# Optimization experiments

Measured on AMD Instinct MI355X. Metric: run time of the kernel, lower is better.

The kernel has to match this reference:

```python
import jax, jax.numpy as jnp
import numpy as np

NEG_SLOPE = 0.2


def gat_conv(x, edge_index, W, a_src, a_dst, b, concat):
    """PyG-style GATConv: add self-loops, linear, edge attention, scatter-softmax, scatter-add."""
    N = x.shape[0]
    H, C = a_src.shape
    loop = jnp.arange(N)
    src = jnp.concatenate([edge_index[0], loop])  # source j (messages flow j -> i)
    dst = jnp.concatenate([edge_index[1], loop])  # target i (aggregation node)
    h = (x @ W).reshape(N, H, C)                  # [N,H,C]
    alpha_s = jnp.sum(h * a_src, axis=-1)         # [N,H]
    alpha_d = jnp.sum(h * a_dst, axis=-1)         # [N,H]
    e = jax.nn.leaky_relu(alpha_s[src] + alpha_d[dst], NEG_SLOPE)  # [E,H]
    # numerically stable scatter-softmax over edges grouped by destination node
    m = jax.ops.segment_max(e, dst, num_segments=N)                # [N,H]
    ex = jnp.exp(e - m[dst])
    denom = jax.ops.segment_sum(ex, dst, num_segments=N)           # [N,H]
    alpha = ex / (denom[dst] + 1e-16)                              # [E,H]
    out = jax.ops.segment_sum(h[src] * alpha[:, :, None], dst, num_segments=N)  # [N,H,C]
    out = out.reshape(N, H * C) if concat else out.mean(axis=1)
    return out + b


def setup_inputs() -> dict:
    key = jax.random.key(0)
    ks = jax.random.split(key, 12)
    N, E, F_IN, HID, OUT, HEADS = 100000, 1600000, 128, 128, 64, 4
    C1 = HID // HEADS
    x = jax.random.normal(ks[0], (N, F_IN), dtype=jnp.float32)
    edge_index = jax.random.randint(ks[1], (2, E), 0, N, dtype=jnp.int64)
    s = 0.05
    return {
        "x": x,
        "edge_index": edge_index,
        "W1": jax.random.normal(ks[2], (F_IN, HEADS * C1), dtype=jnp.float32) * s,
        "a_src1": jax.random.normal(ks[3], (HEADS, C1), dtype=jnp.float32) * s,
        "a_dst1": jax.random.normal(ks[4], (HEADS, C1), dtype=jnp.float32) * s,
        "b1": jnp.zeros((HEADS * C1,), dtype=jnp.float32),
        "W2": jax.random.normal(ks[5], (HID, OUT), dtype=jnp.float32) * s,
        "a_src2": jax.random.normal(ks[6], (1, OUT), dtype=jnp.float32) * s,
        "a_dst2": jax.random.normal(ks[7], (1, OUT), dtype=jnp.float32) * s,
        "b2": jnp.zeros((OUT,), dtype=jnp.float32),
    }


def reference(x, edge_index, W1, a_src1, a_dst1, b1, W2, a_src2, a_dst2, b2):
    h = jax.nn.elu(gat_conv(x, edge_index, W1, a_src1, a_dst1, b1, concat=True))
    # F.dropout(p=0.5, training=False) is the identity in eval mode
    out = gat_conv(h, edge_index, W2, a_src2, a_dst2, b2, concat=False)
    return out
```

## Files before the change

### kernel.cpp

```cpp
#include <hip/hip_runtime.h>
#include <hip/hip_fp16.h>
#include <math.h>
#include <string.h>


#define BSH 9
#define DPB 512
#define NBK 256
#define CH1 16384
#define DBINS 512
#define OCH 1024
#define HB 128
#define LOG2E 1.44269504088896f

using half8 = __attribute__((ext_vector_type(8))) _Float16;
using half4 = __attribute__((ext_vector_type(4))) _Float16;
using floatx4 = __attribute__((ext_vector_type(4))) float;

__device__ __forceinline__ float exp2_fast(float x) {
#if __has_builtin(__builtin_amdgcn_exp2f)
    return __builtin_amdgcn_exp2f(x);
#else
    return exp2f(x);
#endif
}

__device__ __forceinline__ void wfrag(const float* __restrict__ W, __half* __restrict__ WtF,
                                      int NC, int fid) {
    int col = fid & 15, quad = (fid >> 4) & 3, rest = fid >> 6;
    int NT = NC >> 4;
    int t = rest & (NT - 1), k0s = rest / NT;
    int n = t * 16 + col;
    int k = k0s * 32 + quad * 8;
#pragma unroll
    for (int j = 0; j < 8; ++j)
        WtF[fid * 8 + j] = __float2half(W[(k + j) * NC + n]);
}


__global__ __launch_bounds__(256) void bucket_hist(const int* __restrict__ ei, int E, int N,
                                                   unsigned* __restrict__ bcount,
                                                   const float* __restrict__ W1,
                                                   const float* __restrict__ W2,
                                                   __half* __restrict__ WtF1,
                                                   __half* __restrict__ WtF2) {
    if (blockIdx.x >= HB) {
        int tid = (blockIdx.x - HB) * 256 + threadIdx.x;
        if (tid < 2048) wfrag(W1, WtF1, 128, tid);
        else if (tid < 3072) wfrag(W2, WtF2, 64, tid - 2048);
        return;
    }
    __shared__ unsigned hist[NBK];
    int t = threadIdx.x;
    hist[t] = 0;
    __syncthreads();
    int Etot = E + N;
    for (int k = blockIdx.x * 256 + t; k < Etot; k += HB * 256) {
        int d = (k < E) ? ei[E + k] : (k - E);
        atomicAdd(&hist[d >> BSH], 1u);
    }
    __syncthreads();
    unsigned c = hist[t];
    if (c) atomicAdd(&bcount[t], c);
}

__global__ void scan_buckets(const unsigned* __restrict__ bcount, unsigned* __restrict__ bbase,
                             unsigned* __restrict__ bcursor) {
    __shared__ unsigned s[NBK];
    int t = threadIdx.x;
    unsigned v = bcount[t];
    s[t] = v;
    __syncthreads();
    for (int o = 1; o < NBK; o <<= 1) {
        unsigned add = (t >= o) ? s[t - o] : 0;
        __syncthreads();
        s[t] += add;
        __syncthreads();
    }
    unsigned excl = s[t] - v;
    bbase[t] = excl;
    bcursor[t] = excl;
    if (t == NBK - 1) bbase[NBK] = excl + v;
}

__global__ __launch_bounds__(256) void bucket_scatter(const int* __restrict__ ei, int E, int N,
                                                      unsigned* __restrict__ bcursor,
                                                      unsigned* __restrict__ rec) {
    __shared__ unsigned hist[NBK];
    __shared__ unsigned base[NBK];
    int t = threadIdx.x;
    hist[t] = 0;
    __syncthreads();
    int Etot = E + N;
    int k0 = blockIdx.x * CH1;
    int k1 = min(k0 + CH1, Etot);
    for (int k = k0 + t; k < k1; k += 256) {
        int d = (k < E) ? ei[E + k] : (k - E);
        atomicAdd(&hist[d >> BSH], 1u);
    }
    __syncthreads();
    unsigned c = hist[t];
    base[t] = c ? atomicAdd(&bcursor[t], c) : 0u;
    hist[t] = 0;
    __syncthreads();
    for (int k = k0 + t; k < k1; k += 256) {
        int s, d;
        if (k < E) { s = ei[k]; d = ei[E + k]; } else { s = d = k - E; }
        int b = d >> BSH;
        unsigned r = atomicAdd(&hist[b], 1u);
        rec[base[b] + r] = (unsigned)s | ((unsigned)(d & (DPB - 1)) << 17);
    }
}


__global__ __launch_bounds__(256) void bucket_sort(const unsigned* __restrict__ rec,
                                                   const unsigned* __restrict__ bbase,
                                                   int* __restrict__ offs, int* __restrict__ srcs,
                                                   unsigned* __restrict__ deghist,
                                                   unsigned* __restrict__ done,
                                                   unsigned* __restrict__ degcur,
                                                   int N, int Etot, int NSB) {
    __shared__ unsigned hist[DPB];
    __shared__ unsigned tsum[256];
    __shared__ unsigned deg_l[DBINS];
    int t = threadIdx.x, bb = blockIdx.x;
    unsigned r0 = bbase[bb], r1 = bbase[bb + 1];
    hist[t] = 0;
    hist[t + 256] = 0;
    deg_l[t] = 0;
    deg_l[t + 256] = 0;
    __syncthreads();
    int dlo = bb << BSH;
    for (unsigned k = r0 + t; k < r1; k += 256) {
        unsigned e = rec[k];
        atomicAdd(&hist[e >> 17], 1u);
    }
    __syncthreads();
    unsigned h0 = hist[2 * t], h1 = hist[2 * t + 1];
    int d0 = dlo + 2 * t;
    if (d0 < N) atomicAdd(&deg_l[min(h0, (unsigned)(DBINS - 1))], 1u);
    if (d0 + 1 < N) atomicAdd(&deg_l[min(h1, (unsigned)(DBINS - 1))], 1u);
    tsum[t] = h0 + h1;
    __syncthreads();
    for (int o = 1; o < 256; o <<= 1) {
        unsigned a = (t >= o) ? tsum[t - o] : 0;
        __syncthreads();
        tsum[t] += a;
        __syncthreads();
    }
    unsigned tb = tsum[t] - (h0 + h1);
    if (d0 < N) offs[d0] = (int)(r0 + tb);
    if (d0 + 1 < N) offs[d0 + 1] = (int)(r0 + tb + h0);
    hist[2 * t] = tb;
    hist[2 * t + 1] = tb + h0;
    __syncthreads();
    for (unsigned k = r0 + t; k < r1; k += 256) {
        unsigned e = rec[k];
        unsigned r = atomicAdd(&hist[e >> 17], 1u);
        srcs[r0 + r] = (int)(e & 0x1FFFFu);
    }
    if (bb == 0 && t == 0) offs[N] = Etot;
    unsigned c0 = deg_l[t], c1 = deg_l[t + 256];
    if (c0) atomicAdd(&deghist[t], c0);
    if (c1) atomicAdd(&deghist[t + 256], c1);
    __threadfence();
    __shared__ bool amlast;
    if (t == 0) amlast = (atomicAdd(done, 1u) == (unsigned)(NSB - 1));
    __syncthreads();
    if (!amlast) return;
    unsigned v0 = atomicAdd(&deghist[t], 0u);
    unsigned v1 = atomicAdd(&deghist[t + 256], 0u);
    deg_l[t] = v0;
    deg_l[t + 256] = v1;
    __syncthreads();
    for (int o = 1; o < DBINS; o <<= 1) {
        unsigned a0 = (t >= o) ? deg_l[t - o] : 0u;
        unsigned a1 = (t + 256 >= o) ? deg_l[t + 256 - o] : 0u;
        __syncthreads();
        deg_l[t] += a0;
        deg_l[t + 256] += a1;
        __syncthreads();
    }
    degcur[t] = deg_l[t] - v0;
    degcur[t + 256] = deg_l[t + 256] - v1;
}


__global__ __launch_bounds__(256) void order_scatter(const int* __restrict__ offs,
                                                     unsigned* __restrict__ degcur,
                                                     int* __restrict__ order, int N) {
    __shared__ unsigned hist[DBINS];
    __shared__ unsigned base[DBINS];
    int t = threadIdx.x;
    hist[t] = 0;
    hist[t + 256] = 0;
    __syncthreads();
    int k0 = blockIdx.x * OCH, k1 = min(k0 + OCH, N);
    for (int k = k0 + t; k < k1; k += 256) {
        int deg = offs[k + 1] - offs[k];
        atomicAdd(&hist[min(deg, DBINS - 1)], 1u);
    }
    __syncthreads();
    for (int i = t; i < DBINS; i += 256) {
        unsigned c = hist[i];
        base[i] = c ? atomicAdd(&degcur[i], c) : 0u;
        hist[i] = 0;
    }
    __syncthreads();
    for (int k = k0 + t; k < k1; k += 256) {
        int deg = offs[k + 1] - offs[k];
        int b = min(deg, DBINS - 1);
        unsigned r = atomicAdd(&hist[b], 1u);
        order[base[b] + r] = k;
    }
}


template <int NC, int H, typename InT>
__global__ __launch_bounds__(256) void gemm_mfma(const InT* __restrict__ A,
                                                 const __half* __restrict__ WtF,
                                                 __half* __restrict__ C,
                                                 const float* __restrict__ a_src,
                                                 const float* __restrict__ a_dst,
                                                 float* __restrict__ as,
                                                 float* __restrict__ ad, int M) {
    constexpr int NT = NC / 16;
    constexpr int TPH = NT / H;
    int wave = threadIdx.x >> 6;
    int lane = threadIdx.x & 63;
    int quad = lane >> 4, col = lane & 15;
    int row0 = blockIdx.x * 64 + wave * 16;
    int arow = row0 + col;
    if (arow >= M) arow = M - 1;
    floatx4 acc[NT] = {};
    const half8* wf = reinterpret_cast<const half8*>(WtF) + lane;
#pragma unroll
    for (int k0s = 0; k0s < 4; ++k0s) {
        int k0 = k0s * 32;
        half8 af;
        if constexpr (sizeof(InT) == 4) {
            const float* ap = (const float*)A + (size_t)arow * 128 + k0 + quad * 8;
            float4 v0 = *reinterpret_cast<const float4*>(ap);
            float4 v1 = *reinterpret_cast<const float4*>(ap + 4);
            af[0] = (_Float16)v0.x; af[1] = (_Float16)v0.y;
            af[2] = (_Float16)v0.z; af[3] = (_Float16)v0.w;
            af[4] = (_Float16)v1.x; af[5] = (_Float16)v1.y;
            af[6] = (_Float16)v1.z; af[7] = (_Float16)v1.w;
        } else {
            af = *reinterpret_cast<const half8*>((const __half*)A + (size_t)arow * 128 + k0 + quad * 8);
        }
#pragma unroll
        for (int t = 0; t < NT; ++t) {
            half8 bf = wf[(k0s * NT + t) * 64];
            acc[t] = __builtin_amdgcn_mfma_f32_16x16x32_f16(af, bf, acc[t], 0, 0, 0);
        }
    }
    float sa[NT], da[NT];
#pragma unroll
    for (int t = 0; t < NT; ++t) {
        sa[t] = a_src[t * 16 + col];
        da[t] = a_dst[t * 16 + col];
    }
    int rbase = row0 + quad * 4;
#pragma unroll
    for (int reg = 0; reg < 4; ++reg) {
        int row = rbase + reg;
        bool live = row < M;
        if (live) {
#pragma unroll
            for (int t = 0; t < NT; ++t)
                C[(size_t)row * NC + t * 16 + col] = __float2half(acc[t][reg]);
        }
#pragma unroll
        for (int h = 0; h < H; ++h) {
            float ps = 0.f, pd = 0.f;
#pragma unroll
            for (int tt = 0; tt < TPH; ++tt) {
                int t = h * TPH + tt;
                ps = fmaf(acc[t][reg], sa[t], ps);
                pd = fmaf(acc[t][reg], da[t], pd);
            }
#pragma unroll
            for (int o = 1; o < 16; o <<= 1) {
                ps += __shfl_xor(ps, o, 64);
                pd += __shfl_xor(pd, o, 64);
            }
            if (col == 0 && live) {
                as[(size_t)row * H + h] = ps * LOG2E;
                ad[(size_t)row * H + h] = pd * LOG2E;
            }
        }
    }
}


template <int CPL>
__device__ __forceinline__ void ldrow(const __half* __restrict__ p, _Float16* f) {
    if constexpr (CPL == 8) {
        half8 v = *reinterpret_cast<const half8*>(p);
#pragma unroll
        for (int c = 0; c < 8; ++c) f[c] = v[c];
    } else {
        half4 v = *reinterpret_cast<const half4*>(p);
#pragma unroll
        for (int c = 0; c < 4; ++c) f[c] = v[c];
    }
}

template <int H, int ROWS, int CW, bool DOELU, typename OutT>
__global__ __launch_bounds__(256) void aggregateQ(const __half* __restrict__ h,
                                                  const float* __restrict__ as,
                                                  const float* __restrict__ ad,
                                                  const int* __restrict__ offs,
                                                  const int* __restrict__ srcs,
                                                  const int* __restrict__ order,
                                                  const float* __restrict__ bias,
                                                  OutT* __restrict__ out, int N) {
    constexpr int CPL = CW / 16;
    unsigned wave = (blockIdx.x * blockDim.x + threadIdx.x) >> 6;
    unsigned lane = threadIdx.x & 63;
    unsigned lig = lane & 15;
    unsigned idx = wave * 4u + (lane >> 4);
    bool live = idx < (unsigned)N;
    unsigned nc = (unsigned)order[live ? ((unsigned)N - 1u - idx) : 0u];
    unsigned chan = lig * CPL;
    unsigned head = (chan * H) / ROWS;
    float adv = ad[nc * H + head];
    int e0 = offs[nc], e1 = offs[nc + 1];
    int deg = e1 - e0, e1m1 = e1 - 1;
    int md = deg;
    md = max(md, __shfl_xor(md, 16, 64));
    md = max(md, __shfl_xor(md, 32, 64));
    float accs[CPL] = {};
    float den = 0.f;
    for (int k = 0; k < md; k += 4) {
        int b = e0 + k;
        unsigned j0 = (unsigned)srcs[min(b, e1m1)];
        unsigned j1 = (unsigned)srcs[min(b + 1, e1m1)];
        unsigned j2 = (unsigned)srcs[min(b + 2, e1m1)];
        unsigned j3 = (unsigned)srcs[min(b + 3, e1m1)];
        float t0 = as[j0 * H + head] + adv;
        float t1 = as[j1 * H + head] + adv;
        float t2 = as[j2 * H + head] + adv;
        float t3 = as[j3 * H + head] + adv;
        _Float16 f0[CPL], f1[CPL], f2[CPL], f3[CPL];
        ldrow<CPL>(h + j0 * (unsigned)ROWS + chan, f0);
        ldrow<CPL>(h + j1 * (unsigned)ROWS + chan, f1);
        ldrow<CPL>(h + j2 * (unsigned)ROWS + chan, f2);
        ldrow<CPL>(h + j3 * (unsigned)ROWS + chan, f3);
        float x0 = exp2_fast(fmaxf(t0, 0.2f * t0));
        float x1 = exp2_fast(fmaxf(t1, 0.2f * t1));
        float x2 = exp2_fast(fmaxf(t2, 0.2f * t2));
        float x3 = exp2_fast(fmaxf(t3, 0.2f * t3));
        x0 = (k < deg) ? x0 : 0.f;
        x1 = (k + 1 < deg) ? x1 : 0.f;
        x2 = (k + 2 < deg) ? x2 : 0.f;
        x3 = (k + 3 < deg) ? x3 : 0.f;
#pragma unroll
        for (int c = 0; c < CPL; ++c) accs[c] = fmaf(x0, (float)f0[c], accs[c]);
#pragma unroll
        for (int c = 0; c < CPL; ++c) accs[c] = fmaf(x1, (float)f1[c], accs[c]);
#pragma unroll
        for (int c = 0; c < CPL; ++c) accs[c] = fmaf(x2, (float)f2[c], accs[c]);
#pragma unroll
        for (int c = 0; c < CPL; ++c) accs[c] = fmaf(x3, (float)f3[c], accs[c]);
        den += x0 + x1;
        den += x2 + x3;
    }
    float r = 1.0f / (den + 1e-16f);
    if (!live) return;
    const float* bp = bias + chan;
    float vs[CPL];
#pragma unroll
    for (int c = 0; c < CPL; ++c) {
        float v = accs[c] * r + bp[c];
        if constexpr (DOELU) v = (v > 0.f) ? v : expm1f(v);
        vs[c] = v;
    }
    if constexpr (sizeof(OutT) == 2) {
        __half2 st[CPL / 2];
#pragma unroll
        for (int q = 0; q < CPL / 2; ++q)
            st[q] = __floats2half2_rn(vs[2 * q], vs[2 * q + 1]);
        if constexpr (CPL == 8) {
            uint4 v; memcpy(&v, st, 16);
            *reinterpret_cast<uint4*>((__half*)out + nc * (unsigned)ROWS + chan) = v;
        } else {
            uint2 v; memcpy(&v, st, 8);
            *reinterpret_cast<uint2*>((__half*)out + nc * (unsigned)ROWS + chan) = v;
        }
    } else {
#pragma unroll
        for (int q4 = 0; q4 < CPL; q4 += 4) {
            float4 v = make_float4(vs[q4], vs[q4 + 1], vs[q4 + 2], vs[q4 + 3]);
            *reinterpret_cast<float4*>((float*)out + nc * (unsigned)ROWS + chan + q4) = v;
        }
    }
}


extern "C" void kernel_launch(void* const* d_in, const int* in_sizes, int n_in,
                              void* d_out, int out_size, void* d_ws, size_t ws_size,
                              hipStream_t stream) {
    const float* x      = (const float*)d_in[0];
    const int*   ei     = (const int*)d_in[1];
    const float* W1     = (const float*)d_in[2];
    const float* a_src1 = (const float*)d_in[3];
    const float* a_dst1 = (const float*)d_in[4];
    const float* b1     = (const float*)d_in[5];
    const float* W2     = (const float*)d_in[6];
    const float* a_src2 = (const float*)d_in[7];
    const float* a_dst2 = (const float*)d_in[8];
    const float* b2     = (const float*)d_in[9];
    float* out = (float*)d_out;

    const int N = out_size / 64;
    const int E = in_sizes[1] / 2;
    const int Etot = E + N;

    size_t off = 0;
    auto carve = [&](size_t bytes) -> void* {
        void* p = (char*)d_ws + off;
        off += (bytes + 255) & ~(size_t)255;
        return p;
    };
    __half* h1      = (__half*)carve((size_t)N * 128 * 2);
    __half* hmid    = (__half*)carve((size_t)N * 128 * 2);
    float* as1      = (float*)carve((size_t)N * 4 * 4);
    float* ad1      = (float*)carve((size_t)N * 4 * 4);
    float* as2      = (float*)carve((size_t)N * 4);
    float* ad2      = (float*)carve((size_t)N * 4);
    int*   offs     = (int*)carve((size_t)(N + 1) * 4);
    int*   srcs     = (int*)carve((size_t)Etot * 4);
    unsigned* rec   = (unsigned*)carve((size_t)Etot * 4);
    unsigned* ctrs  = (unsigned*)carve((NBK + DBINS + 8) * 4);
    unsigned* bbase   = (unsigned*)carve((NBK + 1) * 4);
    unsigned* bcursor = (unsigned*)carve(NBK * 4);
    unsigned* degcur  = (unsigned*)carve(DBINS * 4);
    __half* WtF1    = (__half*)carve(128 * 128 * 2);
    __half* WtF2    = (__half*)carve(64 * 128 * 2);
    unsigned* bcount  = ctrs;
    unsigned* deghist = ctrs + NBK;
    unsigned* done    = ctrs + NBK + DBINS;
    int* order      = (int*)rec;
    __half* h2      = h1;

    const int NSB = (N + DPB - 1) / DPB;
    const int GB  = (N + 63) / 64;

    hipMemsetAsync(ctrs, 0, (NBK + DBINS + 8) * sizeof(unsigned), stream);
    bucket_hist<<<HB + 12, 256, 0, stream>>>(ei, E, N, bcount, W1, W2, WtF1, WtF2);
    scan_buckets<<<1, 256, 0, stream>>>(bcount, bbase, bcursor);
    bucket_scatter<<<(Etot + CH1 - 1) / CH1, 256, 0, stream>>>(ei, E, N, bcursor, rec);
    bucket_sort<<<NSB, 256, 0, stream>>>(rec, bbase, offs, srcs, deghist, done, degcur,
                                         N, Etot, NSB);

    order_scatter<<<(N + OCH - 1) / OCH, 256, 0, stream>>>(offs, degcur, order, N);

    gemm_mfma<128, 4, float><<<GB, 256, 0, stream>>>(
        x, WtF1, h1, a_src1, a_dst1, as1, ad1, N);
    aggregateQ<4, 128, 128, true, __half><<<(N + 15) / 16, 256, 0, stream>>>(
        h1, as1, ad1, offs, srcs, order, b1, hmid, N);

    gemm_mfma<64, 1, __half><<<GB, 256, 0, stream>>>(
        hmid, WtF2, h2, a_src2, a_dst2, as2, ad2, N);
    aggregateQ<1, 64, 64, false, float><<<(N + 15) / 16, 256, 0, stream>>>(
        h2, as2, ad2, offs, srcs, order, b2, out, N);
}
```

Measured before the change: 375.4 us.

## Replace global degree sort with per-bucket local degree ordering inside bucket_sort

Drops the global degree histogram, last-block scan and separate order_scatter kernel. Each 512-node bucket now sorts its own nodes by descending degree in shared memory and writes the order directly, and aggregation reads order[idx]. This removes one launch, global atomics and a grid-wide last-block pattern. The trade-off is that degree ordering is only local, so wave-level load balance across heavy and light nodes in aggregation may be weaker.

```diff
diff --git a/kernel.cpp b/kernel.cpp
--- a/kernel.cpp
+++ b/kernel.cpp
@@ -9,7 +9,6 @@
 #define NBK 256
 #define CH1 16384
 #define DBINS 512
-#define OCH 1024
 #define HB 128
 #define LOG2E 1.44269504088896f
 
@@ -116,10 +115,8 @@
 __global__ __launch_bounds__(256) void bucket_sort(const unsigned* __restrict__ rec,
                                                    const unsigned* __restrict__ bbase,
                                                    int* __restrict__ offs, int* __restrict__ srcs,
-                                                   unsigned* __restrict__ deghist,
-                                                   unsigned* __restrict__ done,
-                                                   unsigned* __restrict__ degcur,
-                                                   int N, int Etot, int NSB) {
+                                                   int* __restrict__ order,
+                                                   int N, int Etot) {
     __shared__ unsigned hist[DPB];
     __shared__ unsigned tsum[256];
     __shared__ unsigned deg_l[DBINS];
@@ -138,8 +135,11 @@
     __syncthreads();
     unsigned h0 = hist[2 * t], h1 = hist[2 * t + 1];
     int d0 = dlo + 2 * t;
-    if (d0 < N) atomicAdd(&deg_l[min(h0, (unsigned)(DBINS - 1))], 1u);
-    if (d0 + 1 < N) atomicAdd(&deg_l[min(h1, (unsigned)(DBINS - 1))], 1u);
+    unsigned b0 = DBINS - 1u - min(h0, (unsigned)(DBINS - 1));
+    unsigned b1 = DBINS - 1u - min(h1, (unsigned)(DBINS - 1));
+    unsigned sub0 = 0, sub1 = 0;
+    if (d0 < N) sub0 = atomicAdd(&deg_l[b0], 1u);
+    if (d0 + 1 < N) sub1 = atomicAdd(&deg_l[b1], 1u);
     tsum[t] = h0 + h1;
     __syncthreads();
     for (int o = 1; o < 256; o <<= 1) {
@@ -160,18 +160,10 @@
         srcs[r0 + r] = (int)(e & 0x1FFFFu);
     }
     if (bb == 0 && t == 0) offs[N] = Etot;
+    __syncthreads();
     unsigned c0 = deg_l[t], c1 = deg_l[t + 256];
-    if (c0) atomicAdd(&deghist[t], c0);
-    if (c1) atomicAdd(&deghist[t + 256], c1);
-    __threadfence();
-    __shared__ bool amlast;
-    if (t == 0) amlast = (atomicAdd(done, 1u) == (unsigned)(NSB - 1));
-    __syncthreads();
-    if (!amlast) return;
-    unsigned v0 = atomicAdd(&deghist[t], 0u);
-    unsigned v1 = atomicAdd(&deghist[t + 256], 0u);
-    deg_l[t] = v0;
-    deg_l[t + 256] = v1;
+    hist[t] = c0;
+    hist[t + 256] = c1;
     __syncthreads();
     for (int o = 1; o < DBINS; o <<= 1) {
         unsigned a0 = (t >= o) ? deg_l[t - o] : 0u;
@@ -181,38 +173,8 @@
         deg_l[t + 256] += a1;
         __syncthreads();
     }
-    degcur[t] = deg_l[t] - v0;
-    degcur[t + 256] = deg_l[t + 256] - v1;
-}
-
-
-__global__ __launch_bounds__(256) void order_scatter(const int* __restrict__ offs,
-                                                     unsigned* __restrict__ degcur,
-                                                     int* __restrict__ order, int N) {
-    __shared__ unsigned hist[DBINS];
-    __shared__ unsigned base[DBINS];
-    int t = threadIdx.x;
-    hist[t] = 0;
-    hist[t + 256] = 0;
-    __syncthreads();
-    int k0 = blockIdx.x * OCH, k1 = min(k0 + OCH, N);
-    for (int k = k0 + t; k < k1; k += 256) {
-        int deg = offs[k + 1] - offs[k];
-        atomicAdd(&hist[min(deg, DBINS - 1)], 1u);
-    }
-    __syncthreads();
-    for (int i = t; i < DBINS; i += 256) {
-        unsigned c = hist[i];
-        base[i] = c ? atomicAdd(&degcur[i], c) : 0u;
-        hist[i] = 0;
-    }
-    __syncthreads();
-    for (int k = k0 + t; k < k1; k += 256) {
-        int deg = offs[k + 1] - offs[k];
-        int b = min(deg, DBINS - 1);
-        unsigned r = atomicAdd(&hist[b], 1u);
-        order[base[b] + r] = k;
-    }
+    if (d0 < N) order[dlo + (int)(deg_l[b0] - hist[b0] + sub0)] = d0;
+    if (d0 + 1 < N) order[dlo + (int)(deg_l[b1] - hist[b1] + sub1)] = d0 + 1;
 }
 
 
@@ -322,7 +284,7 @@
     unsigned lig = lane & 15;
     unsigned idx = wave * 4u + (lane >> 4);
     bool live = idx < (unsigned)N;
-    unsigned nc = (unsigned)order[live ? ((unsigned)N - 1u - idx) : 0u];
+    unsigned nc = (unsigned)order[live ? idx : 0u];
     unsigned chan = lig * CPL;
     unsigned head = (chan * H) / ROWS;
     float adv = ad[nc * H + head];
@@ -433,29 +395,22 @@
     int*   offs     = (int*)carve((size_t)(N + 1) * 4);
     int*   srcs     = (int*)carve((size_t)Etot * 4);
     unsigned* rec   = (unsigned*)carve((size_t)Etot * 4);
-    unsigned* ctrs  = (unsigned*)carve((NBK + DBINS + 8) * 4);
+    int*   order    = (int*)carve((size_t)N * 4);
+    unsigned* bcount  = (unsigned*)carve(NBK * 4);
     unsigned* bbase   = (unsigned*)carve((NBK + 1) * 4);
     unsigned* bcursor = (unsigned*)carve(NBK * 4);
-    unsigned* degcur  = (unsigned*)carve(DBINS * 4);
     __half* WtF1    = (__half*)carve(128 * 128 * 2);
     __half* WtF2    = (__half*)carve(64 * 128 * 2);
-    unsigned* bcount  = ctrs;
-    unsigned* deghist = ctrs + NBK;
-    unsigned* done    = ctrs + NBK + DBINS;
-    int* order      = (int*)rec;
     __half* h2      = h1;
 
     const int NSB = (N + DPB - 1) / DPB;
     const int GB  = (N + 63) / 64;
 
-    hipMemsetAsync(ctrs, 0, (NBK + DBINS + 8) * sizeof(unsigned), stream);
+    hipMemsetAsync(bcount, 0, NBK * sizeof(unsigned), stream);
     bucket_hist<<<HB + 12, 256, 0, stream>>>(ei, E, N, bcount, W1, W2, WtF1, WtF2);
     scan_buckets<<<1, 256, 0, stream>>>(bcount, bbase, bcursor);
     bucket_scatter<<<(Etot + CH1 - 1) / CH1, 256, 0, stream>>>(ei, E, N, bcursor, rec);
-    bucket_sort<<<NSB, 256, 0, stream>>>(rec, bbase, offs, srcs, deghist, done, degcur,
-                                         N, Etot, NSB);
-
-    order_scatter<<<(N + OCH - 1) / OCH, 256, 0, stream>>>(offs, degcur, order, N);
+    bucket_sort<<<NSB, 256, 0, stream>>>(rec, bbase, offs, srcs, order, N, Etot);
 
     gemm_mfma<128, 4, float><<<GB, 256, 0, stream>>>(
         x, WtF1, h1, a_src1, a_dst1, as1, ad1, N);
```

After: 370.2 us. Within noise of the previous version (-1.4%).
